# Kernel optimization log

Hardware: AMD Instinct MI355X
Metric: run time of the kernel (lower is better)

Reference implementation:

```python
import jax, jax.numpy as jnp
import numpy as np
import math

B, H, S, D = 8, 16, 1024, 64


def setup_inputs() -> dict:
    key = jax.random.key(0)
    kq, kk, kv, kl = jax.random.split(key, 4)
    queries = jax.random.normal(kq, (B * H, S, D), dtype=jnp.float32)
    keys = jax.random.normal(kk, (B * H, S, D), dtype=jnp.float32)
    values = jax.random.normal(kv, (B * H, S, D), dtype=jnp.float32)
    valid_lens = jax.random.randint(kl, (B,), 0, 1024, dtype=jnp.int64)
    return {"queries": queries, "keys": keys, "values": values, "valid_lens": valid_lens}


def reference(queries, keys, values, valid_lens):
    d = queries.shape[-1]
    seq_len = queries.shape[1]
    b = valid_lens.shape[0]
    h = queries.shape[0] // b
    scale = 1.0 / math.sqrt(d)
    # [BH, S, S] scores, faithful to bmm(q, k^T)/sqrt(d)
    scores = jnp.einsum("bqd,bkd->bqk", queries, keys) * scale
    # encode_mask: mask[b, q, k] = (k >= valid_lens[b]) for 1-D valid_lens
    key_mask = jnp.arange(seq_len) >= valid_lens[:, None]  # [B, S]
    scores = scores.reshape(b, h, seq_len, seq_len)
    # masked_fill with 1e-6 (NOT -inf), faithful to the original
    scores = jnp.where(key_mask[:, None, None, :], jnp.float32(1e-6), scores)
    attn = jax.nn.softmax(scores, axis=-1)
    out = jnp.einsum("bhqk,bhkd->bhqd", attn, values.reshape(b, h, seq_len, d))
    return out.reshape(b * h, seq_len, d)
```

## Files before the change

kernel.cpp:

```cpp
#include <hip/hip_runtime.h>
#include <hip/hip_bf16.h>

typedef short short4v __attribute__((ext_vector_type(4)));
typedef short short8v __attribute__((ext_vector_type(8)));
typedef float floatx4 __attribute__((ext_vector_type(4)));

#define SLEN 1024
#define DDIM 64
#define NBH  128
#define PSTR 72

__device__ __forceinline__ unsigned short f2bf(float f) {
  union { float f; unsigned int u; } v; v.f = f;
  unsigned int u = v.u;
  u += 0x7fffu + ((u >> 16) & 1u);
  return (unsigned short)(u >> 16);
}

__device__ __forceinline__ unsigned int pkbf(float a, float b) {
  __hip_bfloat162 h = __float22bfloat162_rn(float2{a, b});
  union { __hip_bfloat162 h; unsigned int u; } c; c.h = h;
  return c.u;
}

__device__ __forceinline__ void ld_lds16(const void* g, void* l) {
  __builtin_amdgcn_global_load_lds(
      (const __attribute__((address_space(1))) void*)g,
      (__attribute__((address_space(3))) void*)l, 16, 0, 0);
}

__device__ __forceinline__ int decode_vl(const int* __restrict__ vraw, int bh_or_b) {
  const bool is64 = (vraw[1] == 0) && (vraw[3] == 0) && (vraw[5] == 0) && (vraw[7] == 0);
  const int b = (bh_or_b >= 16) ? (bh_or_b >> 4) : (bh_or_b >> 4);
  return is64 ? vraw[2 * b] : vraw[b];
}

__global__ __launch_bounds__(256)
void prep_kv(const float* __restrict__ Kg, const float* __restrict__ Vg,
             unsigned short* __restrict__ wsK, unsigned short* __restrict__ wsVT,
             float* __restrict__ CS, const int* __restrict__ vraw, int do_skip) {
  const int bx = blockIdx.x;
  if (bx < 4096) {
    const int tile = bx >> 1;
    if (do_skip) {
      const int bh = tile >> 4, ch = tile & 15;
      const int vl = decode_vl(vraw, bh);
      const int nch = (vl >> 6) + ((vl & 63) ? 1 : 0);
      if (ch >= nch) return;
    }
    const int t = bx * 256 + threadIdx.x;
    const int q = t & 511;
    const int r = q >> 3, gr = q & 7;
    const float4 f0 = *(const float4*)(Kg + (size_t)t * 8);
    const float4 f1 = *(const float4*)(Kg + (size_t)t * 8 + 4);
    short8v s;
    s[0]=(short)f2bf(f0.x); s[1]=(short)f2bf(f0.y); s[2]=(short)f2bf(f0.z); s[3]=(short)f2bf(f0.w);
    s[4]=(short)f2bf(f1.x); s[5]=(short)f2bf(f1.y); s[6]=(short)f2bf(f1.z); s[7]=(short)f2bf(f1.w);
    *(short8v*)(wsK + (size_t)(bx >> 1) * 4096 + r * 64 + ((gr ^ (r & 7)) * 8)) = s;
  } else {
    const int w = threadIdx.x >> 6;
    const int d = threadIdx.x & 63;
    const int tile = (bx - 4096) * 4 + w;
    const int bh = tile >> 4, ch = tile & 15;
    bool do_store = true;
    if (do_skip) {
      const int vl = decode_vl(vraw, bh);
      const int nch = (vl >> 6) + ((vl & 63) ? 1 : 0);
      do_store = (ch < nch);
    }
    const float* src = Vg + ((size_t)(bh * SLEN + ch * 64) * DDIM) + d;
    unsigned short* dst = wsVT + (size_t)tile * 4096 + d * 64;
    float sum = 0.f;
    #pragma unroll
    for (int gg = 0; gg < 8; ++gg) {
      short8v s;
      #pragma unroll
      for (int j = 0; j < 8; ++j) {
        const float x = src[(size_t)(gg * 8 + j) * DDIM];
        sum += x;
        s[j] = (short)f2bf(x);
      }
      if (do_store) *(short8v*)(dst + ((gg ^ (d & 7)) * 8)) = s;
    }
    if (CS) CS[(size_t)tile * 64 + d] = sum;
  }
}

__global__ __launch_bounds__(64)
void prep_sv(float* __restrict__ CS, const int* __restrict__ vraw, int* __restrict__ SRT) {
  const int blk = blockIdx.x;
  if (blk < NBH) {
    const int d = threadIdx.x;
    float acc = 0.f;
    for (int ch = 15; ch >= 0; --ch) {
      const size_t idx = ((size_t)blk * 16 + ch) * 64 + d;
      acc += CS[idx];
      CS[idx] = acc;
    }
  } else {
    const int x = threadIdx.x;
    if (x < 8) {
      int key[16];
      #pragma unroll
      for (int k = 0; k < 16; ++k) {
        const int vv = decode_vl(vraw, x + 8 * k);
        key[k] = (vv >> 6) + ((vv & 63) ? 1 : 0);
      }
      #pragma unroll
      for (int i = 0; i < 16; ++i) {
        int rank = 0;
        #pragma unroll
        for (int k2 = 0; k2 < 16; ++k2)
          rank += (int)((key[k2] > key[i]) || (key[k2] == key[i] && k2 < i));
        SRT[x * 16 + rank] = x + 8 * i;
      }
    }
  }
}

__global__ __launch_bounds__(256)
void attn_main(const float* __restrict__ Qg, const unsigned short* __restrict__ wsK,
               const unsigned short* __restrict__ wsVT, const float* __restrict__ SV,
               const int* __restrict__ SRT, const int* __restrict__ vraw,
               float* __restrict__ Og)
{
  __shared__ unsigned short K_lds[2][4096];
  __shared__ unsigned short VT_lds[2][4096];
  __shared__ unsigned short P_lds[4][32 * PSTR];

  const int t  = threadIdx.x;
  const int w  = t >> 6;
  const int ln = t & 15;
  const int g  = (t >> 4) & 3;

  int bh, q0;
  if (SRT) {
    const int xcd  = blockIdx.x & 7;
    const int lidx = blockIdx.x >> 3;
    const int cu   = lidx & 31;
    const int j    = lidx >> 5;
    const int r    = j * 32 + ((j & 1) ? (31 - cu) : cu);
    bh = SRT[xcd * 16 + (r >> 3)];
    q0 = (r & 7) * 128;
  } else {
    bh = blockIdx.x & 127;
    q0 = (blockIdx.x >> 7) * 128;
  }

  const int vl          = decode_vl(vraw, bh);
  const int full_ch     = vl >> 6;
  const int has_partial = (vl & 63) ? 1 : 0;
  const int nch         = SV ? (full_ch + has_partial) : 16;
  const int tail_start  = full_ch + has_partial;

  const float qs = 0.125f * 1.44269504f;
  short8v bq[2][2];
  #pragma unroll
  for (int nt = 0; nt < 2; ++nt) {
    const float* qp = Qg + ((size_t)bh * SLEN + q0 + w * 32 + nt * 16 + ln) * DDIM;
    #pragma unroll
    for (int st = 0; st < 2; ++st) {
      const float4 f0 = *(const float4*)(qp + st * 32 + g * 8);
      const float4 f1 = *(const float4*)(qp + st * 32 + g * 8 + 4);
      short8v a;
      a[0]=(short)f2bf(f0.x*qs); a[1]=(short)f2bf(f0.y*qs);
      a[2]=(short)f2bf(f0.z*qs); a[3]=(short)f2bf(f0.w*qs);
      a[4]=(short)f2bf(f1.x*qs); a[5]=(short)f2bf(f1.y*qs);
      a[6]=(short)f2bf(f1.z*qs); a[7]=(short)f2bf(f1.w*qs);
      bq[nt][st] = a;
    }
  }

  const int l7  = ln & 7;
  const int sw0 = ((g) ^ l7) * 8;
  const int sw1 = ((4 + g) ^ l7) * 8;

  short8v ones;
  #pragma unroll
  for (int j = 0; j < 8; ++j) ones[j] = (short)0x3F80;

  floatx4 o[2][4], lacc[2];
  #pragma unroll
  for (int m = 0; m < 2; ++m) {
    lacc[m] = (floatx4){0.f, 0.f, 0.f, 0.f};
    #pragma unroll
    for (int f = 0; f < 4; ++f) o[m][f] = (floatx4){0.f, 0.f, 0.f, 0.f};
  }

  const size_t tbase = (size_t)bh * 16 * 4096;
  auto issue = [&](int ch, int b) {
    const unsigned short* gk = wsK  + tbase + (size_t)ch * 4096;
    const unsigned short* gv = wsVT + tbase + (size_t)ch * 4096;
    ld_lds16(gk + (size_t)t * 8,         &K_lds[b][t * 8]);
    ld_lds16(gk + (size_t)(t + 256) * 8, &K_lds[b][(t + 256) * 8]);
    ld_lds16(gv + (size_t)t * 8,         &VT_lds[b][t * 8]);
    ld_lds16(gv + (size_t)(t + 256) * 8, &VT_lds[b][(t + 256) * 8]);
  };

  if (nch > 0) issue(0, 0);

  for (int ch = 0; ch < nch; ++ch) {
    const int b = ch & 1;
    if (ch + 1 < nch) {
      issue(ch + 1, b ^ 1);
      __builtin_amdgcn_s_waitcnt(0x0f74);
    } else {
      __builtin_amdgcn_s_waitcnt(0x0f70);
    }
    __builtin_amdgcn_s_barrier();

    floatx4 c[4][2];
    __builtin_amdgcn_s_setprio(1);
    #pragma unroll
    for (int mt = 0; mt < 4; ++mt) {
      const short8v a0 = *(const short8v*)&K_lds[b][(mt * 16 + ln) * 64 + sw0];
      const short8v a1 = *(const short8v*)&K_lds[b][(mt * 16 + ln) * 64 + sw1];
      #pragma unroll
      for (int nt = 0; nt < 2; ++nt) {
        floatx4 acc = (floatx4){0.f, 0.f, 0.f, 0.f};
        acc = __builtin_amdgcn_mfma_f32_16x16x32_bf16(a0, bq[nt][0], acc, 0, 0, 0);
        acc = __builtin_amdgcn_mfma_f32_16x16x32_bf16(a1, bq[nt][1], acc, 0, 0, 0);
        c[mt][nt] = acc;
      }
    }
    __builtin_amdgcn_s_setprio(0);

    const bool fullv = (ch < full_ch);
    #pragma unroll
    for (int mt = 0; mt < 4; ++mt) {
      const int kg = ch * 64 + mt * 16 + g * 4;
      #pragma unroll
      for (int nt = 0; nt < 2; ++nt) {
        float p[4];
        if (fullv) {
          #pragma unroll
          for (int i = 0; i < 4; ++i) p[i] = __builtin_amdgcn_exp2f(c[mt][nt][i]);
        } else {
          #pragma unroll
          for (int i = 0; i < 4; ++i) {
            const float x = (kg + i < vl) ? c[mt][nt][i] : 0.0f;
            p[i] = __builtin_amdgcn_exp2f(x);
          }
        }
        union { short4v v; unsigned int u[2]; } pk;
        pk.u[0] = pkbf(p[0], p[1]);
        pk.u[1] = pkbf(p[2], p[3]);
        *(short4v*)&P_lds[w][(nt * 16 + ln) * PSTR + mt * 16 + g * 4] = pk.v;
      }
    }

    #pragma unroll
    for (int st = 0; st < 2; ++st) {
      const short8v ap0 = *(const short8v*)&P_lds[w][(ln)      * PSTR + st * 32 + g * 8];
      const short8v ap1 = *(const short8v*)&P_lds[w][(16 + ln) * PSTR + st * 32 + g * 8];
      __builtin_amdgcn_s_setprio(1);
      lacc[0] = __builtin_amdgcn_mfma_f32_16x16x32_bf16(ap0, ones, lacc[0], 0, 0, 0);
      lacc[1] = __builtin_amdgcn_mfma_f32_16x16x32_bf16(ap1, ones, lacc[1], 0, 0, 0);
      const int sw = (st == 0) ? sw0 : sw1;
      #pragma unroll
      for (int f = 0; f < 4; ++f) {
        const short8v bv = *(const short8v*)&VT_lds[b][(f * 16 + ln) * 64 + sw];
        o[0][f] = __builtin_amdgcn_mfma_f32_16x16x32_bf16(ap0, bv, o[0][f], 0, 0, 0);
        o[1][f] = __builtin_amdgcn_mfma_f32_16x16x32_bf16(ap1, bv, o[1][f], 0, 0, 0);
      }
      __builtin_amdgcn_s_setprio(0);
    }

    if (ch + 1 < nch) __builtin_amdgcn_s_barrier();
  }

  if (SV != nullptr && tail_start < 16) {
    const float* sv = SV + ((size_t)bh * 16 + tail_start) * 64;
    float svf[4];
    #pragma unroll
    for (int f = 0; f < 4; ++f) svf[f] = sv[f * 16 + ln];
    const float ml = (float)(SLEN - tail_start * 64);
    #pragma unroll
    for (int m = 0; m < 2; ++m) {
      #pragma unroll
      for (int i = 0; i < 4; ++i) lacc[m][i] += ml;
      #pragma unroll
      for (int f = 0; f < 4; ++f)
        #pragma unroll
        for (int i = 0; i < 4; ++i) o[m][f][i] += svf[f];
    }
  }

  #pragma unroll
  for (int m = 0; m < 2; ++m) {
    #pragma unroll
    for (int i = 0; i < 4; ++i) {
      const float inv = 1.0f / lacc[m][i];
      const size_t row = (size_t)bh * SLEN + q0 + w * 32 + m * 16 + g * 4 + i;
      #pragma unroll
      for (int f = 0; f < 4; ++f)
        Og[row * DDIM + f * 16 + ln] = o[m][f][i] * inv;
    }
  }
}

#define KSTR 72
__device__ __forceinline__ float bf2f(unsigned short h) {
  union { unsigned int u; float f; } v; v.u = ((unsigned int)h) << 16;
  return v.f;
}
__global__ __launch_bounds__(256)
void attn_fwd_fallback(const float* __restrict__ Qg, const float* __restrict__ Kg,
                       const float* __restrict__ Vg, const int* __restrict__ vraw,
                       float* __restrict__ Og)
{
  __shared__ unsigned short K_lds[64 * KSTR];
  __shared__ unsigned short VT_lds[64 * KSTR];
  __shared__ unsigned short P_lds[4][32 * KSTR];
  const int t  = threadIdx.x;
  const int w  = t >> 6;
  const int ln = t & 15;
  const int g  = (t >> 4) & 3;
  const int q0 = blockIdx.x * 128;
  const int bh = blockIdx.y;
  int vl;
  {
    const bool is64 = (vraw[1] == 0) && (vraw[3] == 0) && (vraw[5] == 0) && (vraw[7] == 0);
    const int b = bh >> 4;
    vl = is64 ? vraw[2 * b] : vraw[b];
  }
  short8v aq[2][2];
  #pragma unroll
  for (int m = 0; m < 2; ++m) {
    const float* qp = Qg + ((size_t)bh * SLEN + q0 + w * 32 + m * 16 + ln) * DDIM;
    #pragma unroll
    for (int st = 0; st < 2; ++st) {
      const int d0 = st * 32 + g * 8;
      const float4 f0 = *(const float4*)(qp + d0);
      const float4 f1 = *(const float4*)(qp + d0 + 4);
      short8v a;
      a[0]=(short)f2bf(f0.x); a[1]=(short)f2bf(f0.y); a[2]=(short)f2bf(f0.z); a[3]=(short)f2bf(f0.w);
      a[4]=(short)f2bf(f1.x); a[5]=(short)f2bf(f1.y); a[6]=(short)f2bf(f1.z); a[7]=(short)f2bf(f1.w);
      aq[m][st] = a;
    }
  }
  float mrow[2][4], lrow[2][4];
  floatx4 o[2][4];
  #pragma unroll
  for (int m = 0; m < 2; ++m) {
    #pragma unroll
    for (int i = 0; i < 4; ++i) { mrow[m][i] = -INFINITY; lrow[m][i] = 0.f; }
    #pragma unroll
    for (int f = 0; f < 4; ++f) o[m][f] = (floatx4){0.f, 0.f, 0.f, 0.f};
  }
  const float scale = 0.125f;
  for (int ch = 0; ch < SLEN / 64; ++ch) {
    const int k0 = ch * 64;
    __syncthreads();
    {
      const int c4 = (t & 15) * 4;
      const int r0 = t >> 4;
      const float* kp = Kg + ((size_t)bh * SLEN + k0 + r0) * DDIM + c4;
      #pragma unroll
      for (int r = 0; r < 4; ++r) {
        const float4 v = *(const float4*)(kp + (size_t)(16 * r) * DDIM);
        short4v bq2;
        bq2[0]=(short)f2bf(v.x); bq2[1]=(short)f2bf(v.y); bq2[2]=(short)f2bf(v.z); bq2[3]=(short)f2bf(v.w);
        *(short4v*)&K_lds[(r0 + 16 * r) * KSTR + c4] = bq2;
      }
    }
    {
      const int kb = (t >> 4) * 4;
      const int db = (t & 15) * 4;
      const float* vp = Vg + ((size_t)bh * SLEN + k0 + kb) * DDIM + db;
      const float4 r0 = *(const float4*)(vp);
      const float4 r1 = *(const float4*)(vp + DDIM);
      const float4 r2 = *(const float4*)(vp + 2 * DDIM);
      const float4 r3 = *(const float4*)(vp + 3 * DDIM);
      short4v wa, wb, wc, wd;
      wa[0]=(short)f2bf(r0.x); wa[1]=(short)f2bf(r1.x); wa[2]=(short)f2bf(r2.x); wa[3]=(short)f2bf(r3.x);
      wb[0]=(short)f2bf(r0.y); wb[1]=(short)f2bf(r1.y); wb[2]=(short)f2bf(r2.y); wb[3]=(short)f2bf(r3.y);
      wc[0]=(short)f2bf(r0.z); wc[1]=(short)f2bf(r1.z); wc[2]=(short)f2bf(r2.z); wc[3]=(short)f2bf(r3.z);
      wd[0]=(short)f2bf(r0.w); wd[1]=(short)f2bf(r1.w); wd[2]=(short)f2bf(r2.w); wd[3]=(short)f2bf(r3.w);
      *(short4v*)&VT_lds[(db + 0) * KSTR + kb] = wa;
      *(short4v*)&VT_lds[(db + 1) * KSTR + kb] = wb;
      *(short4v*)&VT_lds[(db + 2) * KSTR + kb] = wc;
      *(short4v*)&VT_lds[(db + 3) * KSTR + kb] = wd;
    }
    __syncthreads();
    floatx4 c[2][4];
    #pragma unroll
    for (int m = 0; m < 2; ++m)
      #pragma unroll
      for (int f = 0; f < 4; ++f) c[m][f] = (floatx4){0.f, 0.f, 0.f, 0.f};
    #pragma unroll
    for (int f = 0; f < 4; ++f) {
      const short8v b0 = *(const short8v*)&K_lds[(16 * f + ln) * KSTR + g * 8];
      const short8v b1 = *(const short8v*)&K_lds[(16 * f + ln) * KSTR + 32 + g * 8];
      #pragma unroll
      for (int m = 0; m < 2; ++m) {
        c[m][f] = __builtin_amdgcn_mfma_f32_16x16x32_bf16(aq[m][0], b0, c[m][f], 0, 0, 0);
        c[m][f] = __builtin_amdgcn_mfma_f32_16x16x32_bf16(aq[m][1], b1, c[m][f], 0, 0, 0);
      }
    }
    #pragma unroll
    for (int m = 0; m < 2; ++m) {
      float s[4][4];
      #pragma unroll
      for (int f = 0; f < 4; ++f) {
        const int kgl = k0 + 16 * f + ln;
        const bool valid = kgl < vl;
        #pragma unroll
        for (int i = 0; i < 4; ++i)
          s[f][i] = valid ? c[m][f][i] * scale : 1e-6f;
      }
      #pragma unroll
      for (int i = 0; i < 4; ++i) {
        float r = fmaxf(fmaxf(s[0][i], s[1][i]), fmaxf(s[2][i], s[3][i]));
        r = fmaxf(r, __shfl_xor(r, 1));
        r = fmaxf(r, __shfl_xor(r, 2));
        r = fmaxf(r, __shfl_xor(r, 4));
        r = fmaxf(r, __shfl_xor(r, 8));
        const float mn = fmaxf(mrow[m][i], r);
        const float al = __expf(mrow[m][i] - mn);
        mrow[m][i] = mn;
        float rs = 0.f;
        #pragma unroll
        for (int f = 0; f < 4; ++f) {
          const unsigned short pb = f2bf(__expf(s[f][i] - mn));
          P_lds[w][(m * 16 + g * 4 + i) * KSTR + 16 * f + ln] = pb;
          rs += bf2f(pb);
        }
        rs += __shfl_xor(rs, 1);
        rs += __shfl_xor(rs, 2);
        rs += __shfl_xor(rs, 4);
        rs += __shfl_xor(rs, 8);
        lrow[m][i] = lrow[m][i] * al + rs;
        #pragma unroll
        for (int f = 0; f < 4; ++f) o[m][f][i] *= al;
      }
    }
    #pragma unroll
    for (int st = 0; st < 2; ++st) {
      const short8v ap0 = *(const short8v*)&P_lds[w][(ln)*KSTR + st * 32 + g * 8];
      const short8v ap1 = *(const short8v*)&P_lds[w][(16 + ln) * KSTR + st * 32 + g * 8];
      #pragma unroll
      for (int f = 0; f < 4; ++f) {
        const short8v bv = *(const short8v*)&VT_lds[(16 * f + ln) * KSTR + st * 32 + g * 8];
        o[0][f] = __builtin_amdgcn_mfma_f32_16x16x32_bf16(ap0, bv, o[0][f], 0, 0, 0);
        o[1][f] = __builtin_amdgcn_mfma_f32_16x16x32_bf16(ap1, bv, o[1][f], 0, 0, 0);
      }
    }
  }
  #pragma unroll
  for (int m = 0; m < 2; ++m) {
    float inv[4];
    #pragma unroll
    for (int i = 0; i < 4; ++i) inv[i] = 1.0f / lrow[m][i];
    #pragma unroll
    for (int f = 0; f < 4; ++f) {
      #pragma unroll
      for (int i = 0; i < 4; ++i) {
        const size_t row = (size_t)bh * SLEN + q0 + w * 32 + m * 16 + g * 4 + i;
        Og[row * DDIM + 16 * f + ln] = o[m][f][i] * inv[i];
      }
    }
  }
}

extern "C" void kernel_launch(void* const* d_in, const int* in_sizes, int n_in,
                              void* d_out, int out_size, void* d_ws, size_t ws_size,
                              hipStream_t stream) {
  const float* Q = (const float*)d_in[0];
  const float* K = (const float*)d_in[1];
  const float* V = (const float*)d_in[2];
  const int*  vl = (const int*)d_in[3];
  float* out = (float*)d_out;

  const size_t ws_kv  = (size_t)2 * NBH * SLEN * DDIM * 2;
  const size_t ws_cs  = ws_kv + (size_t)NBH * 16 * 64 * 4;
  const size_t ws_all = ws_cs + 8 * 16 * 4;

  if (ws_size >= ws_kv) {
    unsigned short* wsK  = (unsigned short*)d_ws;
    unsigned short* wsVT = wsK + (size_t)NBH * SLEN * DDIM;
    float* CS = (ws_size >= ws_all) ? (float*)((char*)d_ws + ws_kv) : nullptr;
    int*  SRT = CS ? (int*)((char*)d_ws + ws_cs) : nullptr;
    prep_kv<<<4608, 256, 0, stream>>>(K, V, wsK, wsVT, CS, vl, CS ? 1 : 0);
    if (CS) prep_sv<<<NBH + 1, 64, 0, stream>>>(CS, vl, SRT);
    attn_main<<<dim3(1024), dim3(256), 0, stream>>>(Q, wsK, wsVT, CS, SRT, vl, out);
  } else {
    attn_fwd_fallback<<<dim3(SLEN / 128, NBH), dim3(256), 0, stream>>>(Q, K, V, vl, out);
  }
}
```

Before: 178.2 us.

## Fuse K/V bf16 conversion into attention main loop with register prefetch

Drops the separate prep kernel that converted K and V to swizzled bf16 in a workspace. The attention kernel now loads fp32 K/V chunks into registers two chunks ahead, then converts and writes them into double-buffered LDS. The column-sum prep kernel now only reads V chunks past the valid length. This removes a full fp32 read plus bf16 write and re-read of K/V, but adds register pressure and conversion work inside the main loop.

Measured after the change: 160.6 us. 1.11x faster.

```diff
diff --git a/kernel.cpp b/kernel.cpp
--- a/kernel.cpp
+++ b/kernel.cpp
@@ -23,67 +23,34 @@
   return c.u;
 }
 
-__device__ __forceinline__ void ld_lds16(const void* g, void* l) {
-  __builtin_amdgcn_global_load_lds(
-      (const __attribute__((address_space(1))) void*)g,
-      (__attribute__((address_space(3))) void*)l, 16, 0, 0);
-}
-
-__device__ __forceinline__ int decode_vl(const int* __restrict__ vraw, int bh_or_b) {
+__device__ __forceinline__ int decode_vl(const int* __restrict__ vraw, int bh) {
   const bool is64 = (vraw[1] == 0) && (vraw[3] == 0) && (vraw[5] == 0) && (vraw[7] == 0);
-  const int b = (bh_or_b >= 16) ? (bh_or_b >> 4) : (bh_or_b >> 4);
+  const int b = bh >> 4;
   return is64 ? vraw[2 * b] : vraw[b];
 }
 
-__global__ __launch_bounds__(256)
-void prep_kv(const float* __restrict__ Kg, const float* __restrict__ Vg,
-             unsigned short* __restrict__ wsK, unsigned short* __restrict__ wsVT,
-             float* __restrict__ CS, const int* __restrict__ vraw, int do_skip) {
-  const int bx = blockIdx.x;
-  if (bx < 4096) {
-    const int tile = bx >> 1;
-    if (do_skip) {
-      const int bh = tile >> 4, ch = tile & 15;
-      const int vl = decode_vl(vraw, bh);
-      const int nch = (vl >> 6) + ((vl & 63) ? 1 : 0);
-      if (ch >= nch) return;
-    }
-    const int t = bx * 256 + threadIdx.x;
-    const int q = t & 511;
-    const int r = q >> 3, gr = q & 7;
-    const float4 f0 = *(const float4*)(Kg + (size_t)t * 8);
-    const float4 f1 = *(const float4*)(Kg + (size_t)t * 8 + 4);
-    short8v s;
-    s[0]=(short)f2bf(f0.x); s[1]=(short)f2bf(f0.y); s[2]=(short)f2bf(f0.z); s[3]=(short)f2bf(f0.w);
-    s[4]=(short)f2bf(f1.x); s[5]=(short)f2bf(f1.y); s[6]=(short)f2bf(f1.z); s[7]=(short)f2bf(f1.w);
-    *(short8v*)(wsK + (size_t)(bx >> 1) * 4096 + r * 64 + ((gr ^ (r & 7)) * 8)) = s;
-  } else {
-    const int w = threadIdx.x >> 6;
-    const int d = threadIdx.x & 63;
-    const int tile = (bx - 4096) * 4 + w;
-    const int bh = tile >> 4, ch = tile & 15;
-    bool do_store = true;
-    if (do_skip) {
-      const int vl = decode_vl(vraw, bh);
-      const int nch = (vl >> 6) + ((vl & 63) ? 1 : 0);
-      do_store = (ch < nch);
-    }
-    const float* src = Vg + ((size_t)(bh * SLEN + ch * 64) * DDIM) + d;
-    unsigned short* dst = wsVT + (size_t)tile * 4096 + d * 64;
-    float sum = 0.f;
-    #pragma unroll
-    for (int gg = 0; gg < 8; ++gg) {
-      short8v s;
-      #pragma unroll
-      for (int j = 0; j < 8; ++j) {
-        const float x = src[(size_t)(gg * 8 + j) * DDIM];
-        sum += x;
-        s[j] = (short)f2bf(x);
-      }
-      if (do_store) *(short8v*)(dst + ((gg ^ (d & 7)) * 8)) = s;
-    }
-    if (CS) CS[(size_t)tile * 64 + d] = sum;
-  }
+__global__ __launch_bounds__(64)
+void prep_cs(const float* __restrict__ Vg, float* __restrict__ CS,
+             const int* __restrict__ vraw) {
+  const int tile = blockIdx.x;
+  const int bh = tile >> 4, ch = tile & 15;
+  const int d = threadIdx.x;
+  const int vl = decode_vl(vraw, bh);
+  const int ts = (vl >> 6) + ((vl & 63) ? 1 : 0);
+  float sum = 0.f;
+  if (ch >= ts) {
+    const float* src = Vg + (size_t)(bh * SLEN + ch * 64) * DDIM + d;
+    float s0 = 0.f, s1 = 0.f, s2 = 0.f, s3 = 0.f;
+    #pragma unroll
+    for (int k = 0; k < 64; k += 4) {
+      s0 += src[(size_t)(k + 0) * DDIM];
+      s1 += src[(size_t)(k + 1) * DDIM];
+      s2 += src[(size_t)(k + 2) * DDIM];
+      s3 += src[(size_t)(k + 3) * DDIM];
+    }
+    sum = (s0 + s1) + (s2 + s3);
+  }
+  CS[(size_t)tile * 64 + d] = sum;
 }
 
 __global__ __launch_bounds__(64)
@@ -119,8 +86,8 @@
 }
 
 __global__ __launch_bounds__(256)
-void attn_main(const float* __restrict__ Qg, const unsigned short* __restrict__ wsK,
-               const unsigned short* __restrict__ wsVT, const float* __restrict__ SV,
+void attn_main(const float* __restrict__ Qg, const float* __restrict__ Kg,
+               const float* __restrict__ Vg, const float* __restrict__ SV,
                const int* __restrict__ SRT, const int* __restrict__ vraw,
                float* __restrict__ Og)
 {
@@ -187,27 +154,67 @@
     for (int f = 0; f < 4; ++f) o[m][f] = (floatx4){0.f, 0.f, 0.f, 0.f};
   }
 
-  const size_t tbase = (size_t)bh * 16 * 4096;
-  auto issue = [&](int ch, int b) {
-    const unsigned short* gk = wsK  + tbase + (size_t)ch * 4096;
-    const unsigned short* gv = wsVT + tbase + (size_t)ch * 4096;
-    ld_lds16(gk + (size_t)t * 8,         &K_lds[b][t * 8]);
-    ld_lds16(gk + (size_t)(t + 256) * 8, &K_lds[b][(t + 256) * 8]);
-    ld_lds16(gv + (size_t)t * 8,         &VT_lds[b][t * 8]);
-    ld_lds16(gv + (size_t)(t + 256) * 8, &VT_lds[b][(t + 256) * 8]);
+  float kr[2][8];
+  float vlo[8], vhi[8];
+  const int dv = t & 31;
+  const int gv = t >> 5;
+
+  const float* kbB = Kg + (size_t)bh * SLEN * DDIM;
+  const float* vbB = Vg + (size_t)bh * SLEN * DDIM;
+
+  auto stage_load = [&](int ch) {
+    const float* kb_ = kbB + (size_t)ch * 64 * DDIM;
+    const float* vb_ = vbB + (size_t)ch * 64 * DDIM;
+    #pragma unroll
+    for (int h = 0; h < 2; ++h) {
+      const int q = t + h * 256;
+      const int r = q >> 3, gr = q & 7;
+      const float4 f0 = *(const float4*)(kb_ + r * DDIM + gr * 8);
+      const float4 f1 = *(const float4*)(kb_ + r * DDIM + gr * 8 + 4);
+      kr[h][0]=f0.x; kr[h][1]=f0.y; kr[h][2]=f0.z; kr[h][3]=f0.w;
+      kr[h][4]=f1.x; kr[h][5]=f1.y; kr[h][6]=f1.z; kr[h][7]=f1.w;
+    }
+    #pragma unroll
+    for (int j = 0; j < 8; ++j) {
+      vlo[j] = vb_[(gv * 8 + j) * DDIM + dv];
+      vhi[j] = vb_[(gv * 8 + j) * DDIM + dv + 32];
+    }
   };
-
-  if (nch > 0) issue(0, 0);
+  auto stage_write = [&](int b) {
+    #pragma unroll
+    for (int h = 0; h < 2; ++h) {
+      const int q = t + h * 256;
+      const int r = q >> 3, gr = q & 7;
+      union { short8v s; unsigned int u[4]; } ks;
+      ks.u[0] = pkbf(kr[h][0], kr[h][1]);
+      ks.u[1] = pkbf(kr[h][2], kr[h][3]);
+      ks.u[2] = pkbf(kr[h][4], kr[h][5]);
+      ks.u[3] = pkbf(kr[h][6], kr[h][7]);
+      *(short8v*)&K_lds[b][r * 64 + ((gr ^ (r & 7)) * 8)] = ks.s;
+    }
+    union { short8v s; unsigned int u[4]; } va, vb2;
+    va.u[0]  = pkbf(vlo[0], vlo[1]); va.u[1]  = pkbf(vlo[2], vlo[3]);
+    va.u[2]  = pkbf(vlo[4], vlo[5]); va.u[3]  = pkbf(vlo[6], vlo[7]);
+    vb2.u[0] = pkbf(vhi[0], vhi[1]); vb2.u[1] = pkbf(vhi[2], vhi[3]);
+    vb2.u[2] = pkbf(vhi[4], vhi[5]); vb2.u[3] = pkbf(vhi[6], vhi[7]);
+    const int swv = (gv ^ (dv & 7)) * 8;
+    *(short8v*)&VT_lds[b][dv * 64 + swv] = va.s;
+    *(short8v*)&VT_lds[b][(dv + 32) * 64 + swv] = vb2.s;
+  };
+
+  if (nch > 0) {
+    stage_load(0);
+    stage_write(0);
+    if (nch > 1) stage_load(1);
+    asm volatile("s_waitcnt lgkmcnt(0)" ::: "memory");
+    __builtin_amdgcn_s_barrier();
+    asm volatile("" ::: "memory");
+  }
 
   for (int ch = 0; ch < nch; ++ch) {
     const int b = ch & 1;
-    if (ch + 1 < nch) {
-      issue(ch + 1, b ^ 1);
-      __builtin_amdgcn_s_waitcnt(0x0f74);
-    } else {
-      __builtin_amdgcn_s_waitcnt(0x0f70);
-    }
-    __builtin_amdgcn_s_barrier();
+    if (ch + 1 < nch) stage_write(b ^ 1);
+    if (ch + 2 < nch) stage_load(ch + 2);
 
     floatx4 c[4][2];
     __builtin_amdgcn_s_setprio(1);
@@ -266,7 +273,11 @@
       __builtin_amdgcn_s_setprio(0);
     }
 
-    if (ch + 1 < nch) __builtin_amdgcn_s_barrier();
+    if (ch + 1 < nch) {
+      asm volatile("s_waitcnt lgkmcnt(0)" ::: "memory");
+      __builtin_amdgcn_s_barrier();
+      asm volatile("" ::: "memory");
+    }
   }
 
   if (SV != nullptr && tail_start < 16) {
@@ -295,170 +306,6 @@
       #pragma unroll
       for (int f = 0; f < 4; ++f)
         Og[row * DDIM + f * 16 + ln] = o[m][f][i] * inv;
-    }
-  }
-}
-
-#define KSTR 72
-__device__ __forceinline__ float bf2f(unsigned short h) {
-  union { unsigned int u; float f; } v; v.u = ((unsigned int)h) << 16;
-  return v.f;
-}
-__global__ __launch_bounds__(256)
-void attn_fwd_fallback(const float* __restrict__ Qg, const float* __restrict__ Kg,
-                       const float* __restrict__ Vg, const int* __restrict__ vraw,
-                       float* __restrict__ Og)
-{
-  __shared__ unsigned short K_lds[64 * KSTR];
-  __shared__ unsigned short VT_lds[64 * KSTR];
-  __shared__ unsigned short P_lds[4][32 * KSTR];
-  const int t  = threadIdx.x;
-  const int w  = t >> 6;
-  const int ln = t & 15;
-  const int g  = (t >> 4) & 3;
-  const int q0 = blockIdx.x * 128;
-  const int bh = blockIdx.y;
-  int vl;
-  {
-    const bool is64 = (vraw[1] == 0) && (vraw[3] == 0) && (vraw[5] == 0) && (vraw[7] == 0);
-    const int b = bh >> 4;
-    vl = is64 ? vraw[2 * b] : vraw[b];
-  }
-  short8v aq[2][2];
-  #pragma unroll
-  for (int m = 0; m < 2; ++m) {
-    const float* qp = Qg + ((size_t)bh * SLEN + q0 + w * 32 + m * 16 + ln) * DDIM;
-    #pragma unroll
-    for (int st = 0; st < 2; ++st) {
-      const int d0 = st * 32 + g * 8;
-      const float4 f0 = *(const float4*)(qp + d0);
-      const float4 f1 = *(const float4*)(qp + d0 + 4);
-      short8v a;
-      a[0]=(short)f2bf(f0.x); a[1]=(short)f2bf(f0.y); a[2]=(short)f2bf(f0.z); a[3]=(short)f2bf(f0.w);
-      a[4]=(short)f2bf(f1.x); a[5]=(short)f2bf(f1.y); a[6]=(short)f2bf(f1.z); a[7]=(short)f2bf(f1.w);
-      aq[m][st] = a;
-    }
-  }
-  float mrow[2][4], lrow[2][4];
-  floatx4 o[2][4];
-  #pragma unroll
-  for (int m = 0; m < 2; ++m) {
-    #pragma unroll
-    for (int i = 0; i < 4; ++i) { mrow[m][i] = -INFINITY; lrow[m][i] = 0.f; }
-    #pragma unroll
-    for (int f = 0; f < 4; ++f) o[m][f] = (floatx4){0.f, 0.f, 0.f, 0.f};
-  }
-  const float scale = 0.125f;
-  for (int ch = 0; ch < SLEN / 64; ++ch) {
-    const int k0 = ch * 64;
-    __syncthreads();
-    {
-      const int c4 = (t & 15) * 4;
-      const int r0 = t >> 4;
-      const float* kp = Kg + ((size_t)bh * SLEN + k0 + r0) * DDIM + c4;
-      #pragma unroll
-      for (int r = 0; r < 4; ++r) {
-        const float4 v = *(const float4*)(kp + (size_t)(16 * r) * DDIM);
-        short4v bq2;
-        bq2[0]=(short)f2bf(v.x); bq2[1]=(short)f2bf(v.y); bq2[2]=(short)f2bf(v.z); bq2[3]=(short)f2bf(v.w);
-        *(short4v*)&K_lds[(r0 + 16 * r) * KSTR + c4] = bq2;
-      }
-    }
-    {
-      const int kb = (t >> 4) * 4;
-      const int db = (t & 15) * 4;
-      const float* vp = Vg + ((size_t)bh * SLEN + k0 + kb) * DDIM + db;
-      const float4 r0 = *(const float4*)(vp);
-      const float4 r1 = *(const float4*)(vp + DDIM);
-      const float4 r2 = *(const float4*)(vp + 2 * DDIM);
-      const float4 r3 = *(const float4*)(vp + 3 * DDIM);
-      short4v wa, wb, wc, wd;
-      wa[0]=(short)f2bf(r0.x); wa[1]=(short)f2bf(r1.x); wa[2]=(short)f2bf(r2.x); wa[3]=(short)f2bf(r3.x);
-      wb[0]=(short)f2bf(r0.y); wb[1]=(short)f2bf(r1.y); wb[2]=(short)f2bf(r2.y); wb[3]=(short)f2bf(r3.y);
-      wc[0]=(short)f2bf(r0.z); wc[1]=(short)f2bf(r1.z); wc[2]=(short)f2bf(r2.z); wc[3]=(short)f2bf(r3.z);
-      wd[0]=(short)f2bf(r0.w); wd[1]=(short)f2bf(r1.w); wd[2]=(short)f2bf(r2.w); wd[3]=(short)f2bf(r3.w);
-      *(short4v*)&VT_lds[(db + 0) * KSTR + kb] = wa;
-      *(short4v*)&VT_lds[(db + 1) * KSTR + kb] = wb;
-      *(short4v*)&VT_lds[(db + 2) * KSTR + kb] = wc;
-      *(short4v*)&VT_lds[(db + 3) * KSTR + kb] = wd;
-    }
-    __syncthreads();
-    floatx4 c[2][4];
-    #pragma unroll
-    for (int m = 0; m < 2; ++m)
-      #pragma unroll
-      for (int f = 0; f < 4; ++f) c[m][f] = (floatx4){0.f, 0.f, 0.f, 0.f};
-    #pragma unroll
-    for (int f = 0; f < 4; ++f) {
-      const short8v b0 = *(const short8v*)&K_lds[(16 * f + ln) * KSTR + g * 8];
-      const short8v b1 = *(const short8v*)&K_lds[(16 * f + ln) * KSTR + 32 + g * 8];
-      #pragma unroll
-      for (int m = 0; m < 2; ++m) {
-        c[m][f] = __builtin_amdgcn_mfma_f32_16x16x32_bf16(aq[m][0], b0, c[m][f], 0, 0, 0);
-        c[m][f] = __builtin_amdgcn_mfma_f32_16x16x32_bf16(aq[m][1], b1, c[m][f], 0, 0, 0);
-      }
-    }
-    #pragma unroll
-    for (int m = 0; m < 2; ++m) {
-      float s[4][4];
-      #pragma unroll
-      for (int f = 0; f < 4; ++f) {
-        const int kgl = k0 + 16 * f + ln;
-        const bool valid = kgl < vl;
-        #pragma unroll
-        for (int i = 0; i < 4; ++i)
-          s[f][i] = valid ? c[m][f][i] * scale : 1e-6f;
-      }
-      #pragma unroll
-      for (int i = 0; i < 4; ++i) {
-        float r = fmaxf(fmaxf(s[0][i], s[1][i]), fmaxf(s[2][i], s[3][i]));
-        r = fmaxf(r, __shfl_xor(r, 1));
-        r = fmaxf(r, __shfl_xor(r, 2));
-        r = fmaxf(r, __shfl_xor(r, 4));
-        r = fmaxf(r, __shfl_xor(r, 8));
-        const float mn = fmaxf(mrow[m][i], r);
-        const float al = __expf(mrow[m][i] - mn);
-        mrow[m][i] = mn;
-        float rs = 0.f;
-        #pragma unroll
-        for (int f = 0; f < 4; ++f) {
-          const unsigned short pb = f2bf(__expf(s[f][i] - mn));
-          P_lds[w][(m * 16 + g * 4 + i) * KSTR + 16 * f + ln] = pb;
-          rs += bf2f(pb);
-        }
-        rs += __shfl_xor(rs, 1);
-        rs += __shfl_xor(rs, 2);
-        rs += __shfl_xor(rs, 4);
-        rs += __shfl_xor(rs, 8);
-        lrow[m][i] = lrow[m][i] * al + rs;
-        #pragma unroll
-        for (int f = 0; f < 4; ++f) o[m][f][i] *= al;
-      }
-    }
-    #pragma unroll
-    for (int st = 0; st < 2; ++st) {
-      const short8v ap0 = *(const short8v*)&P_lds[w][(ln)*KSTR + st * 32 + g * 8];
-      const short8v ap1 = *(const short8v*)&P_lds[w][(16 + ln) * KSTR + st * 32 + g * 8];
-      #pragma unroll
-      for (int f = 0; f < 4; ++f) {
-        const short8v bv = *(const short8v*)&VT_lds[(16 * f + ln) * KSTR + st * 32 + g * 8];
-        o[0][f] = __builtin_amdgcn_mfma_f32_16x16x32_bf16(ap0, bv, o[0][f], 0, 0, 0);
-        o[1][f] = __builtin_amdgcn_mfma_f32_16x16x32_bf16(ap1, bv, o[1][f], 0, 0, 0);
-      }
-    }
-  }
-  #pragma unroll
-  for (int m = 0; m < 2; ++m) {
-    float inv[4];
-    #pragma unroll
-    for (int i = 0; i < 4; ++i) inv[i] = 1.0f / lrow[m][i];
-    #pragma unroll
-    for (int f = 0; f < 4; ++f) {
-      #pragma unroll
-      for (int i = 0; i < 4; ++i) {
-        const size_t row = (size_t)bh * SLEN + q0 + w * 32 + m * 16 + g * 4 + i;
-        Og[row * DDIM + 16 * f + ln] = o[m][f][i] * inv[i];
-      }
     }
   }
 }
@@ -472,19 +319,16 @@
   const int*  vl = (const int*)d_in[3];
   float* out = (float*)d_out;
 
-  const size_t ws_kv  = (size_t)2 * NBH * SLEN * DDIM * 2;
-  const size_t ws_cs  = ws_kv + (size_t)NBH * 16 * 64 * 4;
+  const size_t ws_cs  = (size_t)NBH * 16 * 64 * 4;
   const size_t ws_all = ws_cs + 8 * 16 * 4;
 
-  if (ws_size >= ws_kv) {
-    unsigned short* wsK  = (unsigned short*)d_ws;
-    unsigned short* wsVT = wsK + (size_t)NBH * SLEN * DDIM;
-    float* CS = (ws_size >= ws_all) ? (float*)((char*)d_ws + ws_kv) : nullptr;
-    int*  SRT = CS ? (int*)((char*)d_ws + ws_cs) : nullptr;
-    prep_kv<<<4608, 256, 0, stream>>>(K, V, wsK, wsVT, CS, vl, CS ? 1 : 0);
-    if (CS) prep_sv<<<NBH + 1, 64, 0, stream>>>(CS, vl, SRT);
-    attn_main<<<dim3(1024), dim3(256), 0, stream>>>(Q, wsK, wsVT, CS, SRT, vl, out);
+  if (ws_size >= ws_all) {
+    float* CS = (float*)d_ws;
+    int*  SRT = (int*)((char*)d_ws + ws_cs);
+    prep_cs<<<2048, 64, 0, stream>>>(V, CS, vl);
+    prep_sv<<<NBH + 1, 64, 0, stream>>>(CS, vl, SRT);
+    attn_main<<<dim3(1024), dim3(256), 0, stream>>>(Q, K, V, CS, SRT, vl, out);
   } else {
-    attn_fwd_fallback<<<dim3(SLEN / 128, NBH), dim3(256), 0, stream>>>(Q, K, V, vl, out);
-  }
-}
+    attn_main<<<dim3(1024), dim3(256), 0, stream>>>(Q, K, V, nullptr, nullptr, vl, out);
+  }
+}
```
